# Optimization experiments

Measured on AMD Instinct MI355X. Metric: run time of the kernel, lower is better.

Reference implementation:

```python
import jax, jax.numpy as jnp
import numpy as np

B, S, HID = 1, 2048, 2048
H, KVH, HD = 16, 8, 128
LAMBDA_INIT = 0.2  # lambda_init_fn(depth=0) = 0.8 - 0.6*exp(0)
SCALE = HD ** -0.5
EPS = 1e-5


def rotate_half(x):
    h = x.shape[-1] // 2
    return jnp.concatenate([-x[..., h:], x[..., :h]], axis=-1)


def setup_inputs() -> dict:
    key = jax.random.key(0)
    ks = jax.random.split(key, 12)
    def nrm(k, shape, s=0.02):
        return jax.random.normal(k, shape, dtype=jnp.float32) * s
    d = {}
    d["X"] = jax.random.normal(ks[0], (B, S, HID), dtype=jnp.float32)
    # RoPE tables, shape [B, S, HD]
    pos = jnp.arange(S, dtype=jnp.float32)
    inv_freq = 1.0 / (10000.0 ** (jnp.arange(0, HD, 2, dtype=jnp.float32) / HD))
    freqs = pos[:, None] * inv_freq[None, :]
    emb = jnp.concatenate([freqs, freqs], axis=-1)
    d["cos"] = jnp.broadcast_to(jnp.cos(emb)[None], (B, S, HD)).astype(jnp.float32)
    d["sin"] = jnp.broadcast_to(jnp.sin(emb)[None], (B, S, HD)).astype(jnp.float32)
    d["Wq"] = nrm(ks[1], (H * HD, HID));      d["bq"] = jnp.zeros((H * HD,), jnp.float32)
    d["Wk"] = nrm(ks[2], (KVH * HD, HID));    d["bk"] = jnp.zeros((KVH * HD,), jnp.float32)
    d["Wqn"] = nrm(ks[3], (H * HD, HID));     d["bqn"] = jnp.zeros((H * HD,), jnp.float32)
    d["Wkn"] = nrm(ks[4], (KVH * HD, HID));   d["bkn"] = jnp.zeros((KVH * HD,), jnp.float32)
    d["Wv"] = nrm(ks[5], (2 * KVH * HD, HID)); d["bv"] = jnp.zeros((2 * KVH * HD,), jnp.float32)
    d["Wo"] = nrm(ks[6], (H * HD, 2 * HID));  d["bo"] = jnp.zeros((H * HD,), jnp.float32)
    d["lq1"] = nrm(ks[7], (H, HD), 0.1)
    d["lk1"] = nrm(ks[8], (H, HD), 0.1)
    d["lq2"] = nrm(ks[9], (H, HD), 0.1)
    d["lk2"] = nrm(ks[10], (H, HD), 0.1)
    d["gamma"] = jnp.ones((HD,), jnp.float32)
    d["beta"] = jnp.zeros((HD,), jnp.float32)
    return d


def reference(X, cos, sin, Wq, bq, Wk, bk, Wqn, bqn, Wkn, bkn, Wv, bv, Wo, bo,
              lq1, lk1, lq2, lk2, gamma, beta):
    bsz, q_len, _ = X.shape
    # projections -> [B, H, S, hd]
    q = (X @ Wq.T + bq).reshape(bsz, q_len, H, HD).transpose(0, 2, 1, 3)
    k = (X @ Wk.T + bk).reshape(bsz, q_len, KVH, HD).transpose(0, 2, 1, 3)
    qn = (X @ Wqn.T + bqn).reshape(bsz, q_len, H, HD).transpose(0, 2, 1, 3)
    kn = (X @ Wkn.T + bkn).reshape(bsz, q_len, KVH, HD).transpose(0, 2, 1, 3)
    v = (X @ Wv.T + bv).reshape(bsz, q_len, KVH, 2 * HD).transpose(0, 2, 1, 3)
    # RoPE (broadcast over heads)
    c, s = cos[:, None, :, :], sin[:, None, :, :]
    q = q * c + rotate_half(q) * s
    k = k * c + rotate_half(k) * s
    qn = qn * c + rotate_half(qn) * s
    kn = kn * c + rotate_half(kn) * s
    # GQA repeat
    rep = H // KVH
    k = jnp.repeat(k, rep, axis=1)
    kn = jnp.repeat(kn, rep, axis=1)
    v = jnp.repeat(v, rep, axis=1)
    # dual attention branches
    aw = jnp.einsum('bhqd,bhkd->bhqk', q, k) * SCALE
    an = jnp.einsum('bhqd,bhkd->bhqk', qn, kn) * SCALE
    lam = jnp.exp(jnp.sum(lq1 * lk1, axis=-1)) - jnp.exp(jnp.sum(lq2 * lk2, axis=-1)) + LAMBDA_INIT  # [H]
    attn = jax.nn.softmax(aw, axis=-1) - lam[None, :, None, None] * jax.nn.softmax(an, axis=-1)
    out = jnp.einsum('bhqk,bhkd->bhqd', attn, v)  # [B, H, S, 2*hd]
    # faithful torch .view: raw reshape of contiguous [B,H,S,2hd] -> [B*H*2, hd, S]
    y = out.reshape(bsz * H * 2, HD, q_len)
    mu = jnp.mean(y, axis=(1, 2), keepdims=True)
    var = jnp.mean((y - mu) ** 2, axis=(1, 2), keepdims=True)
    y = (y - mu) / jnp.sqrt(var + EPS)
    y = y * gamma[None, :, None] + beta[None, :, None]
    y = y.reshape(bsz, H, q_len, 2 * HD) * (1.0 - LAMBDA_INIT)
    y = y.transpose(0, 2, 1, 3).reshape(bsz, q_len, 2 * H * HD)
    output = y @ Wo.T + bo
    return output, attn
```

## Files before the change

### kernel.cpp

```cpp
#include <hip/hip_runtime.h>


typedef short bf16x8 __attribute__((ext_vector_type(8)));
typedef float f32x4  __attribute__((ext_vector_type(4)));
typedef unsigned short u16;

#define SLEN 2048
#define HID  2048
#define NH   16
#define NKVH 8
#define HDQ  128
#define DV   256
#define QK_SCALE 0.08838834764831845f
#define LAMB_INIT 0.2f

__device__ __forceinline__ u16 f2bf(float x) {
  unsigned int u = __float_as_uint(x);
  u = (u + 0x7fffu + ((u >> 16) & 1u)) >> 16;
  return (u16)u;
}
__device__ __forceinline__ float bf2f(u16 h) {
  return __uint_as_float(((unsigned int)h) << 16);
}

__device__ __forceinline__ void stage16(const void* g, void* l) {
  __builtin_amdgcn_global_load_lds((__attribute__((address_space(1))) void*)(void*)g,
                                   (__attribute__((address_space(3))) void*)l, 16, 0, 0);
}

__global__ __launch_bounds__(256) void k_cvt(const float* __restrict__ src,
                                             u16* __restrict__ dst, int n) {
  int i = (blockIdx.x * 256 + threadIdx.x) * 4;
  if (i >= n) return;
  float4 v = *(const float4*)(src + i);
  *(ushort4*)(dst + i) = make_ushort4(f2bf(v.x), f2bf(v.y), f2bf(v.z), f2bf(v.w));
}

__global__ __launch_bounds__(64) void k_lam(const float* __restrict__ lq1, const float* __restrict__ lk1,
                                            const float* __restrict__ lq2, const float* __restrict__ lk2,
                                            float* __restrict__ lam) {
  int h = blockIdx.x, l = threadIdx.x;
  float s1 = lq1[h*HDQ + l]*lk1[h*HDQ + l] + lq1[h*HDQ + 64 + l]*lk1[h*HDQ + 64 + l];
  float s2 = lq2[h*HDQ + l]*lk2[h*HDQ + l] + lq2[h*HDQ + 64 + l]*lk2[h*HDQ + 64 + l];
#pragma unroll
  for (int o = 1; o < 64; o <<= 1) { s1 += __shfl_xor(s1, o); s2 += __shfl_xor(s2, o); }
  if (l == 0) lam[h] = __expf(s1) - __expf(s2) + LAMB_INIT;
}

template<int KD>
__device__ __forceinline__ void gemm_core(const u16* __restrict__ A, const u16* __restrict__ B,
                                          int m0, int n0, u16* smem, f32x4 acc[4][4]) {
  u16* As = smem;
  u16* Bs = smem + 8192;
  const int tid = threadIdx.x;
  const int wave = tid >> 6, lane = tid & 63, quad = lane >> 4, l16 = lane & 15;
  const int r0 = (wave & 1) * 64, c0 = (wave >> 1) * 64;
  for (int kt = 0; kt < KD; kt += 64) {
#pragma unroll
    for (int i = 0; i < 4; ++i) {
      int li = i * 256 + tid;
      int row = li >> 3, ce = (li & 7) * 8;
      stage16(A + (size_t)(m0 + row) * KD + kt + ce, As + li * 8);
      stage16(B + (size_t)(n0 + row) * KD + kt + ce, Bs + li * 8);
    }
    __syncthreads();
#pragma unroll
    for (int ks = 0; ks < 2; ++ks) {
      bf16x8 a[4], b[4];
#pragma unroll
      for (int i = 0; i < 4; ++i) a[i] = *(const bf16x8*)(As + (r0 + i*16 + l16)*64 + ks*32 + quad*8);
#pragma unroll
      for (int j = 0; j < 4; ++j) b[j] = *(const bf16x8*)(Bs + (c0 + j*16 + l16)*64 + ks*32 + quad*8);
#pragma unroll
      for (int i = 0; i < 4; ++i)
#pragma unroll
        for (int j = 0; j < 4; ++j)
          acc[i][j] = __builtin_amdgcn_mfma_f32_16x16x32_bf16(a[i], b[j], acc[i][j], 0, 0, 0);
    }
    __syncthreads();
  }
}

__global__ __launch_bounds__(256) void k_proj(const u16* __restrict__ Xb, const u16* __restrict__ Wcat,
    const float* __restrict__ bq, const float* __restrict__ bk, const float* __restrict__ bqn,
    const float* __restrict__ bkn, const float* __restrict__ bv,
    const float* __restrict__ cosg, const float* __restrict__ sing,
    u16* __restrict__ Qg, u16* __restrict__ Kg, u16* __restrict__ Qng, u16* __restrict__ Kng,
    u16* __restrict__ Vtg)
{
  __shared__ u16 smem[16384];
  const int m0 = blockIdx.x * 128;
  const int cb = blockIdx.y;
  const int tid = threadIdx.x;
  f32x4 acc[4][4];
  const f32x4 zf = {0.f, 0.f, 0.f, 0.f};
#pragma unroll
  for (int i = 0; i < 4; ++i)
#pragma unroll
    for (int j = 0; j < 4; ++j) acc[i][j] = zf;

  gemm_core<HID>(Xb, Wcat, m0, cb * 128, smem, acc);

  const int wave = tid >> 6, lane = tid & 63, quad = lane >> 4, l16 = lane & 15;
  const int r0 = (wave & 1) * 64, c0 = (wave >> 1) * 64;

  const float* bptr; int cloc;
  if      (cb < 16) { bptr = bq;  cloc = cb * 128; }
  else if (cb < 24) { bptr = bk;  cloc = (cb - 16) * 128; }
  else if (cb < 40) { bptr = bqn; cloc = (cb - 24) * 128; }
  else if (cb < 48) { bptr = bkn; cloc = (cb - 40) * 128; }
  else              { bptr = bv;  cloc = (cb - 48) * 128; }
  float bias[4];
#pragma unroll
  for (int j = 0; j < 4; ++j) bias[j] = bptr[cloc + c0 + j*16 + l16];

#pragma unroll
  for (int i = 0; i < 4; ++i)
#pragma unroll
    for (int j = 0; j < 4; ++j)
#pragma unroll
      for (int reg = 0; reg < 4; ++reg)
        smem[(r0 + i*16 + quad*4 + reg) * 128 + c0 + j*16 + l16] = f2bf(acc[i][j][reg] + bias[j]);
  __syncthreads();

  if (cb < 48) {
    u16* outp; float sc;
    if      (cb < 16) { outp = Qg  + (size_t)cb        * SLEN * HDQ; sc = QK_SCALE; }
    else if (cb < 24) { outp = Kg  + (size_t)(cb - 16) * SLEN * HDQ; sc = 1.f; }
    else if (cb < 40) { outp = Qng + (size_t)(cb - 24) * SLEN * HDQ; sc = QK_SCALE; }
    else              { outp = Kng + (size_t)(cb - 40) * SLEN * HDQ; sc = 1.f; }
    const int r = tid >> 1;
    const int dh = (tid & 1) * 64;
    const int s = m0 + r;
    const float sgn = dh ? 1.f : -1.f;
#pragma unroll
    for (int dc = 0; dc < 64; dc += 4) {
      const int d = dh + dc;
      float4 cv = *(const float4*)(cosg + (size_t)s * HDQ + d);
      float4 sv = *(const float4*)(sing + (size_t)s * HDQ + d);
      float cvals[4] = {cv.x, cv.y, cv.z, cv.w};
      float svals[4] = {sv.x, sv.y, sv.z, sv.w};
      u16 o[4];
#pragma unroll
      for (int t = 0; t < 4; ++t) {
        float x  = bf2f(smem[r * 128 + d + t]);
        float xr = bf2f(smem[r * 128 + ((d + t) ^ 64)]);
        o[t] = f2bf((x * cvals[t] + sgn * xr * svals[t]) * sc);
      }
      *(ushort4*)(outp + (size_t)s * HDQ + d) = make_ushort4(o[0], o[1], o[2], o[3]);
    }
  } else {
    const int kvh = (cb - 48) >> 1;
    const int dvh = ((cb - 48) & 1) * 128;
    const int dvl = tid >> 1;
    const int sc0 = (tid & 1) * 64;
    u16* dst = Vtg + ((size_t)(kvh * DV + dvh + dvl)) * SLEN + m0 + sc0;
#pragma unroll
    for (int u8 = 0; u8 < 8; ++u8) {
      bf16x8 pack;
#pragma unroll
      for (int e = 0; e < 8; ++e) pack[e] = (short)smem[(sc0 + u8*8 + e) * 128 + dvl];
      *(bf16x8*)(dst + u8 * 8) = pack;
    }
  }
}

__global__ __launch_bounds__(256) void k_attn(
    const u16* __restrict__ Qg, const u16* __restrict__ Kg,
    const u16* __restrict__ Qng, const u16* __restrict__ Kng,
    const u16* __restrict__ Vtg, const float* __restrict__ lam,
    float* __restrict__ attn_out, float* __restrict__ Obuf,
    float* __restrict__ gsum, float* __restrict__ gsumsq)
{
  __shared__ u16 Qs[64 * 136];
  __shared__ u16 Qns[64 * 136];
  __shared__ u16 Ps[64 * 72];
  __shared__ float l1s[64], l2s[64];

  const int tid = threadIdx.x;
  const int h = blockIdx.x & 15, qb = blockIdx.x >> 4;
  const int q0 = qb * 64, kvh = h >> 1;
  const u16* Qsrc  = Qg  + ((size_t)h * SLEN + q0) * HDQ;
  const u16* Qnsrc = Qng + ((size_t)h * SLEN + q0) * HDQ;

#pragma unroll
  for (int i = 0; i < 4; ++i) {
    int li = i * 256 + tid;
    int row = li >> 4, col = (li & 15) * 8;
    *(bf16x8*)(Qs  + row * 136 + col) = *(const bf16x8*)(Qsrc  + li * 8);
    *(bf16x8*)(Qns + row * 136 + col) = *(const bf16x8*)(Qnsrc + li * 8);
  }
  if (tid < 64) { l1s[tid] = 0.f; l2s[tid] = 0.f; }
  __syncthreads();

  const int wave = tid >> 6, lane = tid & 63, quad = lane >> 4, l16 = lane & 15;
  const u16* Kb  = Kg  + (size_t)kvh * SLEN * HDQ;
  const u16* Knb = Kng + (size_t)kvh * SLEN * HDQ;
  const f32x4 zf = {0.f, 0.f, 0.f, 0.f};

#define COMPUTE_SSN(Sv, Snv)                                                              \
  {                                                                                       \
    _Pragma("unroll")                                                                     \
    for (int ks = 0; ks < 4; ++ks) {                                                      \
      const bf16x8 bk_  = *(const bf16x8*)(Kb  + (size_t)(cc0 + l16) * HDQ + ks*32 + quad*8); \
      const bf16x8 bkn_ = *(const bf16x8*)(Knb + (size_t)(cc0 + l16) * HDQ + ks*32 + quad*8); \
      _Pragma("unroll")                                                                   \
      for (int m = 0; m < 4; ++m) {                                                       \
        const bf16x8 aq_  = *(const bf16x8*)(Qs  + (m*16 + l16) * 136 + ks*32 + quad*8);  \
        const bf16x8 aqn_ = *(const bf16x8*)(Qns + (m*16 + l16) * 136 + ks*32 + quad*8);  \
        Sv[m]  = __builtin_amdgcn_mfma_f32_16x16x32_bf16(aq_,  bk_,  Sv[m], 0, 0, 0);     \
        Snv[m] = __builtin_amdgcn_mfma_f32_16x16x32_bf16(aqn_, bkn_, Snv[m], 0, 0, 0);    \
      }                                                                                   \
    }                                                                                     \
  }

  float r1[4][4], r2[4][4];
#pragma unroll
  for (int m = 0; m < 4; ++m)
#pragma unroll
    for (int reg = 0; reg < 4; ++reg) { r1[m][reg] = 0.f; r2[m][reg] = 0.f; }

  for (int kb = 0; kb < 32; ++kb) {
    const int cc0 = kb * 64 + wave * 16;
    f32x4 S[4], Sn[4];
#pragma unroll
    for (int m = 0; m < 4; ++m) { S[m] = zf; Sn[m] = zf; }
    COMPUTE_SSN(S, Sn)
#pragma unroll
    for (int m = 0; m < 4; ++m)
#pragma unroll
      for (int reg = 0; reg < 4; ++reg) {
        r1[m][reg] += __expf(S[m][reg]);
        r2[m][reg] += __expf(Sn[m][reg]);
      }
  }
#pragma unroll
  for (int m = 0; m < 4; ++m)
#pragma unroll
    for (int reg = 0; reg < 4; ++reg) {
      float v1 = r1[m][reg], v2 = r2[m][reg];
#pragma unroll
      for (int o = 1; o < 16; o <<= 1) { v1 += __shfl_xor(v1, o); v2 += __shfl_xor(v2, o); }
      if (l16 == 0) {
        atomicAdd(&l1s[m*16 + quad*4 + reg], v1);
        atomicAdd(&l2s[m*16 + quad*4 + reg], v2);
      }
    }
  __syncthreads();

  const float lamh = lam[h];
  float inv1[4][4], inv2[4][4];
#pragma unroll
  for (int m = 0; m < 4; ++m)
#pragma unroll
    for (int reg = 0; reg < 4; ++reg) {
      int row = m*16 + quad*4 + reg;
      inv1[m][reg] = 1.f / l1s[row];
      inv2[m][reg] = lamh / l2s[row];
    }

  f32x4 O[4][4];
#pragma unroll
  for (int m = 0; m < 4; ++m)
#pragma unroll
    for (int n = 0; n < 4; ++n) O[m][n] = zf;

  float* ab = attn_out + ((size_t)h * SLEN + q0) * SLEN;
  const u16* Vb = Vtg + (size_t)(kvh * DV + wave * 64) * SLEN;

  for (int kb = 0; kb < 32; ++kb) {
    const int cc0 = kb * 64 + wave * 16;
    f32x4 S[4], Sn[4];
#pragma unroll
    for (int m = 0; m < 4; ++m) { S[m] = zf; Sn[m] = zf; }
    COMPUTE_SSN(S, Sn)
#pragma unroll
    for (int m = 0; m < 4; ++m)
#pragma unroll
      for (int reg = 0; reg < 4; ++reg) {
        const int row = m*16 + quad*4 + reg;
        float p = __expf(S[m][reg]) * inv1[m][reg] - __expf(Sn[m][reg]) * inv2[m][reg];
        ab[(size_t)row * SLEN + cc0 + l16] = p;
        Ps[row * 72 + wave * 16 + l16] = f2bf(p);
      }
    __syncthreads();
#pragma unroll
    for (int ks = 0; ks < 2; ++ks) {
      bf16x8 a[4];
#pragma unroll
      for (int m = 0; m < 4; ++m) a[m] = *(const bf16x8*)(Ps + (m*16 + l16) * 72 + ks*32 + quad*8);
#pragma unroll
      for (int n = 0; n < 4; ++n) {
        const bf16x8 bv_ = *(const bf16x8*)(Vb + (size_t)(n*16 + l16) * SLEN + kb*64 + ks*32 + quad*8);
#pragma unroll
        for (int m = 0; m < 4; ++m)
          O[m][n] = __builtin_amdgcn_mfma_f32_16x16x32_bf16(a[m], bv_, O[m][n], 0, 0, 0);
      }
    }
    __syncthreads();
  }

  float lsum = 0.f, lsq = 0.f;
#pragma unroll
  for (int m = 0; m < 4; ++m)
#pragma unroll
    for (int n = 0; n < 4; ++n)
#pragma unroll
      for (int reg = 0; reg < 4; ++reg) {
        const int row = m*16 + quad*4 + reg;
        const int dv = wave*64 + n*16 + l16;
        float v = O[m][n][reg];
        Obuf[((size_t)h * SLEN + q0 + row) * DV + dv] = v;
        lsum += v; lsq += v * v;
      }
#pragma unroll
  for (int o = 1; o < 64; o <<= 1) { lsum += __shfl_xor(lsum, o); lsq += __shfl_xor(lsq, o); }
  if (lane == 0) {
    const int g = h * 2 + (q0 >> 10);
    atomicAdd(&gsum[g], lsum);
    atomicAdd(&gsumsq[g], lsq);
  }
#undef COMPUTE_SSN
}

__global__ void k_gfin(const float* __restrict__ gsum, const float* __restrict__ gsumsq,
                       float* __restrict__ mus, float* __restrict__ rstds) {
  int g = threadIdx.x;
  if (g >= 32) return;
  const float N = 262144.f;
  float mu = gsum[g] / N;
  float var = gsumsq[g] / N - mu * mu;
  mus[g] = mu;
  rstds[g] = rsqrtf(var + 1e-5f);
}

__global__ __launch_bounds__(256) void k_norm(const float* __restrict__ Obuf,
    const float* __restrict__ mus, const float* __restrict__ rstds,
    const float* __restrict__ gamma, const float* __restrict__ beta,
    u16* __restrict__ Yb)
{
  const int e = (blockIdx.x * 256 + threadIdx.x) * 4;
  const int h = e >> 19;
  const int rem = e & 524287;
  const int q = rem >> 8;
  const int d = rem & 255;
  const int g = h * 2 + (q >> 10);
  const int c = (q & 1023) >> 3;
  const float mu = mus[g], rs = rstds[g];
  const float gm = gamma[c], bt = beta[c];
  float4 v = *(const float4*)(Obuf + e);
  float vals[4] = {v.x, v.y, v.z, v.w};
  u16 o[4];
#pragma unroll
  for (int t = 0; t < 4; ++t) o[t] = f2bf(((vals[t] - mu) * rs * gm + bt) * 0.8f);
  *(ushort4*)(Yb + (size_t)q * 4096 + h * DV + d) = make_ushort4(o[0], o[1], o[2], o[3]);
}

__global__ __launch_bounds__(256) void k_out(const u16* __restrict__ Yb, const u16* __restrict__ Wob,
                                             const float* __restrict__ bo, float* __restrict__ out)
{
  __shared__ u16 smem[16384];
  const int m0 = blockIdx.x * 128, n0 = blockIdx.y * 128;
  f32x4 acc[4][4];
  const f32x4 zf = {0.f, 0.f, 0.f, 0.f};
#pragma unroll
  for (int i = 0; i < 4; ++i)
#pragma unroll
    for (int j = 0; j < 4; ++j) acc[i][j] = zf;

  gemm_core<4096>(Yb, Wob, m0, n0, smem, acc);

  const int tid = threadIdx.x;
  const int wave = tid >> 6, lane = tid & 63, quad = lane >> 4, l16 = lane & 15;
  const int r0 = (wave & 1) * 64, c0 = (wave >> 1) * 64;
#pragma unroll
  for (int j = 0; j < 4; ++j) {
    const float b = bo[n0 + c0 + j*16 + l16];
#pragma unroll
    for (int i = 0; i < 4; ++i)
#pragma unroll
      for (int reg = 0; reg < 4; ++reg)
        out[(size_t)(m0 + r0 + i*16 + quad*4 + reg) * 2048 + n0 + c0 + j*16 + l16] =
            acc[i][j][reg] + b;
  }
}

extern "C" void kernel_launch(void* const* d_in, const int* in_sizes, int n_in,
                              void* d_out, int out_size, void* d_ws, size_t ws_size,
                              hipStream_t stream) {
  const float* X    = (const float*)d_in[0];
  const float* cosg = (const float*)d_in[1];
  const float* sing = (const float*)d_in[2];
  const float* Wq   = (const float*)d_in[3];
  const float* bq   = (const float*)d_in[4];
  const float* Wk   = (const float*)d_in[5];
  const float* bk   = (const float*)d_in[6];
  const float* Wqn  = (const float*)d_in[7];
  const float* bqn  = (const float*)d_in[8];
  const float* Wkn  = (const float*)d_in[9];
  const float* bkn  = (const float*)d_in[10];
  const float* Wv   = (const float*)d_in[11];
  const float* bv   = (const float*)d_in[12];
  const float* Wo   = (const float*)d_in[13];
  const float* bo   = (const float*)d_in[14];
  const float* lq1  = (const float*)d_in[15];
  const float* lk1  = (const float*)d_in[16];
  const float* lq2  = (const float*)d_in[17];
  const float* lk2  = (const float*)d_in[18];
  const float* gamma= (const float*)d_in[19];
  const float* beta = (const float*)d_in[20];

  float* out0 = (float*)d_out;
  float* attn = out0 + 4194304;

  char* attnB = (char*)attn;
  u16* Xb   = (u16*)(attnB + 0);
  u16* Wcat = (u16*)(attnB + 8388608);

  char* ws = (char*)d_ws;
  u16* Wob   = (u16*)(ws + 0);
  u16* Qg    = (u16*)(ws + 16777216);
  u16* Kgp   = (u16*)(ws + 25165824);
  u16* Qng   = (u16*)(ws + 29360128);
  u16* Kng   = (u16*)(ws + 37748736);
  u16* Vtg   = (u16*)(ws + 41943040);
  float* lam    = (float*)(ws + 50331648);
  float* gsum   = (float*)(ws + 50331776);
  float* gsumsq = (float*)(ws + 50331904);
  float* musv   = (float*)(ws + 50332032);
  float* rstds  = (float*)(ws + 50332160);
  float* Obuf   = (float*)(ws + 50332672);
  u16* Yb       = (u16*)(ws + 83887104);

  hipMemsetAsync(gsum, 0, 64 * sizeof(float), stream);

  k_cvt<<<4096, 256, 0, stream>>>(X,   Xb,               4194304);
  k_cvt<<<4096, 256, 0, stream>>>(Wq,  Wcat,             4194304);
  k_cvt<<<2048, 256, 0, stream>>>(Wk,  Wcat + 4194304,   2097152);
  k_cvt<<<4096, 256, 0, stream>>>(Wqn, Wcat + 6291456,   4194304);
  k_cvt<<<2048, 256, 0, stream>>>(Wkn, Wcat + 10485760,  2097152);
  k_cvt<<<4096, 256, 0, stream>>>(Wv,  Wcat + 12582912,  4194304);
  k_cvt<<<8192, 256, 0, stream>>>(Wo,  Wob,              8388608);
  k_lam<<<16, 64, 0, stream>>>(lq1, lk1, lq2, lk2, lam);

  k_proj<<<dim3(16, 64), 256, 0, stream>>>(Xb, Wcat, bq, bk, bqn, bkn, bv,
                                           cosg, sing, Qg, Kgp, Qng, Kng, Vtg);

  k_attn<<<512, 256, 0, stream>>>(Qg, Kgp, Qng, Kng, Vtg, lam, attn, Obuf, gsum, gsumsq);

  k_gfin<<<1, 32, 0, stream>>>(gsum, gsumsq, musv, rstds);
  k_norm<<<8192, 256, 0, stream>>>(Obuf, musv, rstds, gamma, beta, Yb);
  k_out<<<dim3(16, 16), 256, 0, stream>>>(Yb, Wob, bo, out0);
}
```

Before: 888.4 us.

## Merge conversion launches, halve attention query tile, split-K output GEMM with atomics

Folds the seven fp32-to-bf16 conversion launches into one segmented kernel. Moves the lambda computation into the attention kernel and the group-stat finalisation into the norm kernel, removing two small launches. Halves the attention query tile from 64 to 32 rows, doubling the grid to 1024 blocks with a launch-bounds occupancy hint, which also doubles K/V re-reads. Splits the output GEMM along K into two halves that atomically add into a bias-initialised output, raising block count at the cost of atomic traffic, an extra init pass and non-deterministic summation order.

```diff
diff --git a/kernel.cpp b/kernel.cpp
--- a/kernel.cpp
+++ b/kernel.cpp
@@ -28,26 +28,23 @@
                                    (__attribute__((address_space(3))) void*)l, 16, 0, 0);
 }
 
-__global__ __launch_bounds__(256) void k_cvt(const float* __restrict__ src,
-                                             u16* __restrict__ dst, int n) {
-  int i = (blockIdx.x * 256 + threadIdx.x) * 4;
-  if (i >= n) return;
-  float4 v = *(const float4*)(src + i);
-  *(ushort4*)(dst + i) = make_ushort4(f2bf(v.x), f2bf(v.y), f2bf(v.z), f2bf(v.w));
-}
-
-__global__ __launch_bounds__(64) void k_lam(const float* __restrict__ lq1, const float* __restrict__ lk1,
-                                            const float* __restrict__ lq2, const float* __restrict__ lk2,
-                                            float* __restrict__ lam) {
-  int h = blockIdx.x, l = threadIdx.x;
-  float s1 = lq1[h*HDQ + l]*lk1[h*HDQ + l] + lq1[h*HDQ + 64 + l]*lk1[h*HDQ + 64 + l];
-  float s2 = lq2[h*HDQ + l]*lk2[h*HDQ + l] + lq2[h*HDQ + 64 + l]*lk2[h*HDQ + 64 + l];
-#pragma unroll
-  for (int o = 1; o < 64; o <<= 1) { s1 += __shfl_xor(s1, o); s2 += __shfl_xor(s2, o); }
-  if (l == 0) lam[h] = __expf(s1) - __expf(s2) + LAMB_INIT;
-}
-
-template<int KD>
+struct CvtArgs {
+  const float* src[7];
+  u16* dst[7];
+  int nblk[7];
+};
+
+__global__ __launch_bounds__(256) void k_cvt_all(CvtArgs a) {
+  int b = blockIdx.x, seg = 0;
+#pragma unroll
+  for (int s = 0; s < 6; ++s)
+    if (seg == s && b >= a.nblk[s]) { b -= a.nblk[s]; seg = s + 1; }
+  const int i = (b * 256 + threadIdx.x) * 4;
+  float4 v = *(const float4*)(a.src[seg] + i);
+  *(ushort4*)(a.dst[seg] + i) = make_ushort4(f2bf(v.x), f2bf(v.y), f2bf(v.z), f2bf(v.w));
+}
+
+template<int KD, int LDA>
 __device__ __forceinline__ void gemm_core(const u16* __restrict__ A, const u16* __restrict__ B,
                                           int m0, int n0, u16* smem, f32x4 acc[4][4]) {
   u16* As = smem;
@@ -60,8 +57,8 @@
     for (int i = 0; i < 4; ++i) {
       int li = i * 256 + tid;
       int row = li >> 3, ce = (li & 7) * 8;
-      stage16(A + (size_t)(m0 + row) * KD + kt + ce, As + li * 8);
-      stage16(B + (size_t)(n0 + row) * KD + kt + ce, Bs + li * 8);
+      stage16(A + (size_t)(m0 + row) * LDA + kt + ce, As + li * 8);
+      stage16(B + (size_t)(n0 + row) * LDA + kt + ce, Bs + li * 8);
     }
     __syncthreads();
 #pragma unroll
@@ -99,7 +96,7 @@
 #pragma unroll
     for (int j = 0; j < 4; ++j) acc[i][j] = zf;
 
-  gemm_core<HID>(Xb, Wcat, m0, cb * 128, smem, acc);
+  gemm_core<HID, HID>(Xb, Wcat, m0, cb * 128, smem, acc);
 
   const int wave = tid >> 6, lane = tid & 63, quad = lane >> 4, l16 = lane & 15;
   const int r0 = (wave & 1) * 64, c0 = (wave >> 1) * 64;
@@ -165,32 +162,43 @@
   }
 }
 
-__global__ __launch_bounds__(256) void k_attn(
+__global__ __launch_bounds__(256, 4) void k_attn(
     const u16* __restrict__ Qg, const u16* __restrict__ Kg,
     const u16* __restrict__ Qng, const u16* __restrict__ Kng,
-    const u16* __restrict__ Vtg, const float* __restrict__ lam,
+    const u16* __restrict__ Vtg,
+    const float* __restrict__ lq1, const float* __restrict__ lk1,
+    const float* __restrict__ lq2, const float* __restrict__ lk2,
     float* __restrict__ attn_out, float* __restrict__ Obuf,
     float* __restrict__ gsum, float* __restrict__ gsumsq)
 {
-  __shared__ u16 Qs[64 * 136];
-  __shared__ u16 Qns[64 * 136];
-  __shared__ u16 Ps[64 * 72];
-  __shared__ float l1s[64], l2s[64];
+  __shared__ u16 Qs[32 * 136];
+  __shared__ u16 Qns[32 * 136];
+  __shared__ u16 Ps[32 * 72];
+  __shared__ float l1s[32], l2s[32];
+  __shared__ float lamv;
 
   const int tid = threadIdx.x;
   const int h = blockIdx.x & 15, qb = blockIdx.x >> 4;
-  const int q0 = qb * 64, kvh = h >> 1;
+  const int q0 = qb * 32, kvh = h >> 1;
   const u16* Qsrc  = Qg  + ((size_t)h * SLEN + q0) * HDQ;
   const u16* Qnsrc = Qng + ((size_t)h * SLEN + q0) * HDQ;
 
 #pragma unroll
-  for (int i = 0; i < 4; ++i) {
+  for (int i = 0; i < 2; ++i) {
     int li = i * 256 + tid;
     int row = li >> 4, col = (li & 15) * 8;
     *(bf16x8*)(Qs  + row * 136 + col) = *(const bf16x8*)(Qsrc  + li * 8);
     *(bf16x8*)(Qns + row * 136 + col) = *(const bf16x8*)(Qnsrc + li * 8);
   }
-  if (tid < 64) { l1s[tid] = 0.f; l2s[tid] = 0.f; }
+  if (tid < 64) {
+    float s1 = lq1[h*HDQ + tid]*lk1[h*HDQ + tid] + lq1[h*HDQ + 64 + tid]*lk1[h*HDQ + 64 + tid];
+    float s2 = lq2[h*HDQ + tid]*lk2[h*HDQ + tid] + lq2[h*HDQ + 64 + tid]*lk2[h*HDQ + 64 + tid];
+#pragma unroll
+    for (int o = 1; o < 64; o <<= 1) { s1 += __shfl_xor(s1, o); s2 += __shfl_xor(s2, o); }
+    if (tid == 0) lamv = __expf(s1) - __expf(s2) + LAMB_INIT;
+  } else if (tid < 96) {
+    l1s[tid - 64] = 0.f; l2s[tid - 64] = 0.f;
+  }
   __syncthreads();
 
   const int wave = tid >> 6, lane = tid & 63, quad = lane >> 4, l16 = lane & 15;
@@ -205,7 +213,7 @@
       const bf16x8 bk_  = *(const bf16x8*)(Kb  + (size_t)(cc0 + l16) * HDQ + ks*32 + quad*8); \
       const bf16x8 bkn_ = *(const bf16x8*)(Knb + (size_t)(cc0 + l16) * HDQ + ks*32 + quad*8); \
       _Pragma("unroll")                                                                   \
-      for (int m = 0; m < 4; ++m) {                                                       \
+      for (int m = 0; m < 2; ++m) {                                                       \
         const bf16x8 aq_  = *(const bf16x8*)(Qs  + (m*16 + l16) * 136 + ks*32 + quad*8);  \
         const bf16x8 aqn_ = *(const bf16x8*)(Qns + (m*16 + l16) * 136 + ks*32 + quad*8);  \
         Sv[m]  = __builtin_amdgcn_mfma_f32_16x16x32_bf16(aq_,  bk_,  Sv[m], 0, 0, 0);     \
@@ -214,20 +222,20 @@
     }                                                                                     \
   }
 
-  float r1[4][4], r2[4][4];
-#pragma unroll
-  for (int m = 0; m < 4; ++m)
+  float r1[2][4], r2[2][4];
+#pragma unroll
+  for (int m = 0; m < 2; ++m)
 #pragma unroll
     for (int reg = 0; reg < 4; ++reg) { r1[m][reg] = 0.f; r2[m][reg] = 0.f; }
 
   for (int kb = 0; kb < 32; ++kb) {
     const int cc0 = kb * 64 + wave * 16;
-    f32x4 S[4], Sn[4];
-#pragma unroll
-    for (int m = 0; m < 4; ++m) { S[m] = zf; Sn[m] = zf; }
+    f32x4 S[2], Sn[2];
+#pragma unroll
+    for (int m = 0; m < 2; ++m) { S[m] = zf; Sn[m] = zf; }
     COMPUTE_SSN(S, Sn)
 #pragma unroll
-    for (int m = 0; m < 4; ++m)
+    for (int m = 0; m < 2; ++m)
 #pragma unroll
       for (int reg = 0; reg < 4; ++reg) {
         r1[m][reg] += __expf(S[m][reg]);
@@ -235,7 +243,7 @@
       }
   }
 #pragma unroll
-  for (int m = 0; m < 4; ++m)
+  for (int m = 0; m < 2; ++m)
 #pragma unroll
     for (int reg = 0; reg < 4; ++reg) {
       float v1 = r1[m][reg], v2 = r2[m][reg];
@@ -248,10 +256,10 @@
     }
   __syncthreads();
 
-  const float lamh = lam[h];
-  float inv1[4][4], inv2[4][4];
-#pragma unroll
-  for (int m = 0; m < 4; ++m)
+  const float lamh = lamv;
+  float inv1[2][4], inv2[2][4];
+#pragma unroll
+  for (int m = 0; m < 2; ++m)
 #pragma unroll
     for (int reg = 0; reg < 4; ++reg) {
       int row = m*16 + quad*4 + reg;
@@ -259,9 +267,9 @@
       inv2[m][reg] = lamh / l2s[row];
     }
 
-  f32x4 O[4][4];
-#pragma unroll
-  for (int m = 0; m < 4; ++m)
+  f32x4 O[2][4];
+#pragma unroll
+  for (int m = 0; m < 2; ++m)
 #pragma unroll
     for (int n = 0; n < 4; ++n) O[m][n] = zf;
 
@@ -270,12 +278,12 @@
 
   for (int kb = 0; kb < 32; ++kb) {
     const int cc0 = kb * 64 + wave * 16;
-    f32x4 S[4], Sn[4];
-#pragma unroll
-    for (int m = 0; m < 4; ++m) { S[m] = zf; Sn[m] = zf; }
+    f32x4 S[2], Sn[2];
+#pragma unroll
+    for (int m = 0; m < 2; ++m) { S[m] = zf; Sn[m] = zf; }
     COMPUTE_SSN(S, Sn)
 #pragma unroll
-    for (int m = 0; m < 4; ++m)
+    for (int m = 0; m < 2; ++m)
 #pragma unroll
       for (int reg = 0; reg < 4; ++reg) {
         const int row = m*16 + quad*4 + reg;
@@ -286,14 +294,14 @@
     __syncthreads();
 #pragma unroll
     for (int ks = 0; ks < 2; ++ks) {
-      bf16x8 a[4];
-#pragma unroll
-      for (int m = 0; m < 4; ++m) a[m] = *(const bf16x8*)(Ps + (m*16 + l16) * 72 + ks*32 + quad*8);
+      bf16x8 a[2];
+#pragma unroll
+      for (int m = 0; m < 2; ++m) a[m] = *(const bf16x8*)(Ps + (m*16 + l16) * 72 + ks*32 + quad*8);
 #pragma unroll
       for (int n = 0; n < 4; ++n) {
         const bf16x8 bv_ = *(const bf16x8*)(Vb + (size_t)(n*16 + l16) * SLEN + kb*64 + ks*32 + quad*8);
 #pragma unroll
-        for (int m = 0; m < 4; ++m)
+        for (int m = 0; m < 2; ++m)
           O[m][n] = __builtin_amdgcn_mfma_f32_16x16x32_bf16(a[m], bv_, O[m][n], 0, 0, 0);
       }
     }
@@ -302,7 +310,7 @@
 
   float lsum = 0.f, lsq = 0.f;
 #pragma unroll
-  for (int m = 0; m < 4; ++m)
+  for (int m = 0; m < 2; ++m)
 #pragma unroll
     for (int n = 0; n < 4; ++n)
 #pragma unroll
@@ -323,19 +331,8 @@
 #undef COMPUTE_SSN
 }
 
-__global__ void k_gfin(const float* __restrict__ gsum, const float* __restrict__ gsumsq,
-                       float* __restrict__ mus, float* __restrict__ rstds) {
-  int g = threadIdx.x;
-  if (g >= 32) return;
-  const float N = 262144.f;
-  float mu = gsum[g] / N;
-  float var = gsumsq[g] / N - mu * mu;
-  mus[g] = mu;
-  rstds[g] = rsqrtf(var + 1e-5f);
-}
-
 __global__ __launch_bounds__(256) void k_norm(const float* __restrict__ Obuf,
-    const float* __restrict__ mus, const float* __restrict__ rstds,
+    const float* __restrict__ gsum, const float* __restrict__ gsumsq,
     const float* __restrict__ gamma, const float* __restrict__ beta,
     u16* __restrict__ Yb)
 {
@@ -346,7 +343,10 @@
   const int d = rem & 255;
   const int g = h * 2 + (q >> 10);
   const int c = (q & 1023) >> 3;
-  const float mu = mus[g], rs = rstds[g];
+  const float Ninv = 1.f / 262144.f;
+  const float mu = gsum[g] * Ninv;
+  const float var = gsumsq[g] * Ninv - mu * mu;
+  const float rs = rsqrtf(var + 1e-5f);
   const float gm = gamma[c], bt = beta[c];
   float4 v = *(const float4*)(Obuf + e);
   float vals[4] = {v.x, v.y, v.z, v.w};
@@ -356,11 +356,19 @@
   *(ushort4*)(Yb + (size_t)q * 4096 + h * DV + d) = make_ushort4(o[0], o[1], o[2], o[3]);
 }
 
+__global__ __launch_bounds__(256) void k_out_init(const float* __restrict__ bo,
+                                                  float* __restrict__ out) {
+  const int i = (blockIdx.x * 256 + threadIdx.x) * 4;
+  const int n = i & 2047;
+  *(float4*)(out + i) = *(const float4*)(bo + n);
+}
+
 __global__ __launch_bounds__(256) void k_out(const u16* __restrict__ Yb, const u16* __restrict__ Wob,
-                                             const float* __restrict__ bo, float* __restrict__ out)
+                                             float* __restrict__ out)
 {
   __shared__ u16 smem[16384];
   const int m0 = blockIdx.x * 128, n0 = blockIdx.y * 128;
+  const int z = blockIdx.z;
   f32x4 acc[4][4];
   const f32x4 zf = {0.f, 0.f, 0.f, 0.f};
 #pragma unroll
@@ -368,21 +376,19 @@
 #pragma unroll
     for (int j = 0; j < 4; ++j) acc[i][j] = zf;
 
-  gemm_core<4096>(Yb, Wob, m0, n0, smem, acc);
+  gemm_core<2048, 4096>(Yb + (size_t)z * 2048, Wob + (size_t)z * 2048, m0, n0, smem, acc);
 
   const int tid = threadIdx.x;
   const int wave = tid >> 6, lane = tid & 63, quad = lane >> 4, l16 = lane & 15;
   const int r0 = (wave & 1) * 64, c0 = (wave >> 1) * 64;
 #pragma unroll
-  for (int j = 0; j < 4; ++j) {
-    const float b = bo[n0 + c0 + j*16 + l16];
+  for (int j = 0; j < 4; ++j)
 #pragma unroll
     for (int i = 0; i < 4; ++i)
 #pragma unroll
       for (int reg = 0; reg < 4; ++reg)
-        out[(size_t)(m0 + r0 + i*16 + quad*4 + reg) * 2048 + n0 + c0 + j*16 + l16] =
-            acc[i][j][reg] + b;
-  }
+        atomicAdd(out + (size_t)(m0 + r0 + i*16 + quad*4 + reg) * 2048 + n0 + c0 + j*16 + l16,
+                  acc[i][j][reg]);
 }
 
 extern "C" void kernel_launch(void* const* d_in, const int* in_sizes, int n_in,
@@ -424,31 +430,31 @@
   u16* Qng   = (u16*)(ws + 29360128);
   u16* Kng   = (u16*)(ws + 37748736);
   u16* Vtg   = (u16*)(ws + 41943040);
-  float* lam    = (float*)(ws + 50331648);
-  float* gsum   = (float*)(ws + 50331776);
+  float* gsum   = (float*)(ws + 50331648);
   float* gsumsq = (float*)(ws + 50331904);
-  float* musv   = (float*)(ws + 50332032);
-  float* rstds  = (float*)(ws + 50332160);
   float* Obuf   = (float*)(ws + 50332672);
   u16* Yb       = (u16*)(ws + 83887104);
 
   hipMemsetAsync(gsum, 0, 64 * sizeof(float), stream);
 
-  k_cvt<<<4096, 256, 0, stream>>>(X,   Xb,               4194304);
-  k_cvt<<<4096, 256, 0, stream>>>(Wq,  Wcat,             4194304);
-  k_cvt<<<2048, 256, 0, stream>>>(Wk,  Wcat + 4194304,   2097152);
-  k_cvt<<<4096, 256, 0, stream>>>(Wqn, Wcat + 6291456,   4194304);
-  k_cvt<<<2048, 256, 0, stream>>>(Wkn, Wcat + 10485760,  2097152);
-  k_cvt<<<4096, 256, 0, stream>>>(Wv,  Wcat + 12582912,  4194304);
-  k_cvt<<<8192, 256, 0, stream>>>(Wo,  Wob,              8388608);
-  k_lam<<<16, 64, 0, stream>>>(lq1, lk1, lq2, lk2, lam);
+  CvtArgs ca;
+  ca.src[0] = X;   ca.dst[0] = Xb;               ca.nblk[0] = 4096;
+  ca.src[1] = Wq;  ca.dst[1] = Wcat;             ca.nblk[1] = 4096;
+  ca.src[2] = Wk;  ca.dst[2] = Wcat + 4194304;   ca.nblk[2] = 2048;
+  ca.src[3] = Wqn; ca.dst[3] = Wcat + 6291456;   ca.nblk[3] = 4096;
+  ca.src[4] = Wkn; ca.dst[4] = Wcat + 10485760;  ca.nblk[4] = 2048;
+  ca.src[5] = Wv;  ca.dst[5] = Wcat + 12582912;  ca.nblk[5] = 4096;
+  ca.src[6] = Wo;  ca.dst[6] = Wob;              ca.nblk[6] = 8192;
+  k_cvt_all<<<28672, 256, 0, stream>>>(ca);
+
+  k_out_init<<<4096, 256, 0, stream>>>(bo, out0);
 
   k_proj<<<dim3(16, 64), 256, 0, stream>>>(Xb, Wcat, bq, bk, bqn, bkn, bv,
                                            cosg, sing, Qg, Kgp, Qng, Kng, Vtg);
 
-  k_attn<<<512, 256, 0, stream>>>(Qg, Kgp, Qng, Kng, Vtg, lam, attn, Obuf, gsum, gsumsq);
-
-  k_gfin<<<1, 32, 0, stream>>>(gsum, gsumsq, musv, rstds);
-  k_norm<<<8192, 256, 0, stream>>>(Obuf, musv, rstds, gamma, beta, Yb);
-  k_out<<<dim3(16, 16), 256, 0, stream>>>(Yb, Wob, bo, out0);
-}
+  k_attn<<<1024, 256, 0, stream>>>(Qg, Kgp, Qng, Kng, Vtg, lq1, lk1, lq2, lk2,
+                                   attn, Obuf, gsum, gsumsq);
+
+  k_norm<<<8192, 256, 0, stream>>>(Obuf, gsum, gsumsq, gamma, beta, Yb);
+  k_out<<<dim3(16, 16, 2), 256, 0, stream>>>(Yb, Wob, out0);
+}
```

New measurement: 937.2 us. 1.05x slower.
